# Performance work log

Measured on AMD Instinct MI355X. Metric: run time of the kernel, lower is better.

## Reference

```python
import jax, jax.numpy as jnp
import numpy as np

N_NODES = 50000
N_EDGES = 800000
IN_CH = 128
HEADS = 4
OUT_CH = 32


def setup_inputs() -> dict:
    key = jax.random.key(0)
    k1, k2, k3, k4 = jax.random.split(key, 4)
    x = jax.random.normal(k1, (N_NODES, IN_CH), dtype=jnp.float32)
    edge_index = jax.random.randint(k2, (2, N_EDGES), 0, N_NODES, dtype=jnp.int64)
    # nn.Linear weight [out, in] with xavier-uniform init
    limW = float(np.sqrt(6.0 / (IN_CH + HEADS * OUT_CH)))
    W = jax.random.uniform(k3, (HEADS * OUT_CH, IN_CH), minval=-limW, maxval=limW, dtype=jnp.float32)
    lima = float(np.sqrt(6.0 / (HEADS + 2 * OUT_CH)))
    att = jax.random.uniform(k4, (HEADS, 2 * OUT_CH), minval=-lima, maxval=lima, dtype=jnp.float32)
    bias = jnp.zeros((HEADS * OUT_CH,), dtype=jnp.float32)
    return {"x": x, "edge_index": edge_index, "W": W, "att": att, "bias": bias}


def reference(x, edge_index, W, att, bias):
    n = x.shape[0]
    heads, two_c = att.shape
    out_ch = two_c // 2
    loop = jnp.arange(n, dtype=edge_index.dtype)
    src = jnp.concatenate([edge_index[0], loop])  # [E+n]
    dst = jnp.concatenate([edge_index[1], loop])  # [E+n]
    h = (x @ W.T).reshape(n, heads, out_ch)       # [n, H, C]
    h_src = h[src]                                # [E+n, H, C]
    h_dst = h[dst]                                # [E+n, H, C]
    # e = sum over channels of att applied to [h_src || h_dst]
    e = (jnp.einsum('ehc,hc->eh', h_src, att[:, :out_ch])
         + jnp.einsum('ehc,hc->eh', h_dst, att[:, out_ch:]))  # [E+n, H]
    e = jax.nn.leaky_relu(e, negative_slope=0.2)
    # segment softmax over incoming edges per dst node
    e_max = jax.ops.segment_max(e, dst, num_segments=n)        # [n, H]
    alpha = jnp.exp(e - e_max[dst])                            # [E+n, H]
    a_sum = jax.ops.segment_sum(alpha, dst, num_segments=n)    # [n, H]
    alpha = alpha / jnp.maximum(a_sum[dst], 1e-10)
    weighted = h_src * alpha[..., None]                        # [E+n, H, C]
    out = jax.ops.segment_sum(weighted, dst, num_segments=n)   # [n, H, C]
    out = out.reshape(n, heads * out_ch)                       # concat=True
    return out + bias
```

## Files before the change

kernel.cpp:

```cpp
#include <hip/hip_runtime.h>
#include <hip/hip_bf16.h>
#include <math.h>

#define N_NODES 50000
#define N_EDGES 800000
#define IN_CH   128
#define HEADS   4
#define OUT_CH  32
#define HC      128
#define WROWS   136

#define CB_SHIFT 7
#define CB_NODES 128
#define N_CB     391
#define NBK      128
#define EPB      (N_EDGES / NBK)
#define PCAP     44
#define ND_CAP   48
#define CB_CAP   2560
#define NGB      196

typedef __attribute__((ext_vector_type(8))) short short8;
typedef __attribute__((ext_vector_type(4))) float floatx4;

__device__ __forceinline__ short f2bf(float f) {
    __hip_bfloat16 h = __float2bfloat16(f);
    return *reinterpret_cast<short*>(&h);
}

__global__ __launch_bounds__(256) void kA_fused(
    const int* __restrict__ src, const int* __restrict__ dst,
    unsigned* __restrict__ priv, int* __restrict__ cnt2,
    const float* __restrict__ x, const float* __restrict__ W,
    const float* __restrict__ att, __hip_bfloat16* __restrict__ hbuf,
    float* __restrict__ asrc, float* __restrict__ adst) {

    __shared__ short smem[128 * WROWS];

    const int tid = threadIdx.x;

    if (blockIdx.x < NBK) {
        int* lcnt = (int*)smem;
        const int blk = blockIdx.x;
        for (int i = tid; i < N_CB; i += 256) lcnt[i] = 0;
        __syncthreads();

        const int e0 = blk * EPB;
        for (int e = e0 + tid; e < e0 + EPB; e += 256) {
            int s = src[e];
            int d = dst[e];
            int cb = d >> CB_SHIFT;
            int pos = atomicAdd(&lcnt[cb], 1);
            if (pos < PCAP)
                priv[((size_t)cb * NBK + blk) * PCAP + pos] =
                    ((unsigned)(d & (CB_NODES - 1)) << 16) | (unsigned)s;
        }
        __syncthreads();
        for (int i = tid; i < N_CB; i += 256)
            cnt2[blk * N_CB + i] = min(lcnt[i], PCAP);
        return;
    }

    short* Wlds = smem;
    const int wave = tid >> 6;
    const int lane = tid & 63;
    const int col  = lane & 15;
    const int q    = lane >> 4;

    {
        int row  = tid >> 1;
        int half = tid & 1;
        const float4* Wr = (const float4*)(W + row * IN_CH + half * 64);
        short* dp = Wlds + row * WROWS + half * 64;
#pragma unroll
        for (int i = 0; i < 16; ++i) {
            float4 v = Wr[i];
            ushort4 p;
            p.x = (unsigned short)f2bf(v.x);
            p.y = (unsigned short)f2bf(v.y);
            p.z = (unsigned short)f2bf(v.z);
            p.w = (unsigned short)f2bf(v.w);
            *(ushort4*)(dp + i * 4) = p;
        }
    }

    float attS[8], attD[8];
#pragma unroll
    for (int t = 0; t < 8; ++t) {
        int base = (t >> 1) * 64 + (t & 1) * 16 + col;
        attS[t] = att[base];
        attD[t] = att[base + 32];
    }

    __syncthreads();

    const int node_base = (blockIdx.x - NBK) * 256;

    for (int it = 0; it < 4; ++it) {
        const int node0 = node_base + (it * 4 + wave) * 16;
        const int m  = node0 + col;
        const int mc = min(m, N_NODES - 1);

        floatx4 acc[8];
#pragma unroll
        for (int t = 0; t < 8; ++t) acc[t] = (floatx4){0.f, 0.f, 0.f, 0.f};

#pragma unroll
        for (int ks = 0; ks < 4; ++ks) {
            const float4* xp = (const float4*)(x + (size_t)mc * IN_CH + ks * 32 + q * 8);
            float4 v0 = xp[0];
            float4 v1 = xp[1];
            short8 af;
            af[0] = f2bf(v0.x); af[1] = f2bf(v0.y); af[2] = f2bf(v0.z); af[3] = f2bf(v0.w);
            af[4] = f2bf(v1.x); af[5] = f2bf(v1.y); af[6] = f2bf(v1.z); af[7] = f2bf(v1.w);
#pragma unroll
            for (int t = 0; t < 8; ++t) {
                const short8 bf = *(const short8*)(Wlds + (t * 16 + col) * WROWS + ks * 32 + q * 8);
                acc[t] = __builtin_amdgcn_mfma_f32_16x16x32_bf16(af, bf, acc[t], 0, 0, 0);
            }
        }

#pragma unroll
        for (int r = 0; r < 4; ++r) {
            const int node = node0 + q * 4 + r;
            const bool valid = node < N_NODES;
            float hs[4] = {0.f, 0.f, 0.f, 0.f};
            float hd[4] = {0.f, 0.f, 0.f, 0.f};
#pragma unroll
            for (int t = 0; t < 8; ++t) {
                float v = acc[t][r];
                if (valid) hbuf[(size_t)node * HC + t * 16 + col] = __float2bfloat16(v);
                hs[t >> 1] = fmaf(v, attS[t], hs[t >> 1]);
                hd[t >> 1] = fmaf(v, attD[t], hd[t >> 1]);
            }
#pragma unroll
            for (int off = 8; off; off >>= 1) {
#pragma unroll
                for (int h = 0; h < 4; ++h) {
                    hs[h] += __shfl_down(hs[h], off, 16);
                    hd[h] += __shfl_down(hd[h], off, 16);
                }
            }
            if (col == 0 && valid) {
#pragma unroll
                for (int h = 0; h < 4; ++h) {
                    asrc[node * HEADS + h] = hs[h];
                    adst[node * HEADS + h] = hd[h];
                }
            }
        }
    }
}

__global__ __launch_bounds__(256) void kc2_bin(
    const int* __restrict__ cnt2, const unsigned* __restrict__ priv,
    unsigned short* __restrict__ csr16, unsigned* __restrict__ meta) {

    __shared__ unsigned short list[CB_NODES * ND_CAP];
    __shared__ int lcnt[CB_NODES];
    __shared__ int ccnt[CB_NODES];
    __shared__ int lpre[CB_NODES];
    __shared__ int lcnt2[NBK];

    const int b   = blockIdx.x;
    const int tid = threadIdx.x;
    const int node0 = b << CB_SHIFT;
    const int nInB  = min(CB_NODES, N_NODES - node0);

    if (tid < CB_NODES) lcnt[tid] = 0;
    if (tid < NBK) lcnt2[tid] = cnt2[tid * N_CB + b];
    __syncthreads();

    const unsigned* p = priv + (size_t)b * NBK * PCAP;
    for (int idx = tid; idx < NBK * PCAP; idx += 256) {
        int blk = (idx * 5958) >> 18;
        int j   = idx - blk * PCAP;
        if (j < lcnt2[blk]) {
            unsigned ent = p[idx];
            int dl   = ent >> 16;
            int slot = atomicAdd(&lcnt[dl], 1);
            if (slot < ND_CAP) list[dl * ND_CAP + slot] = (unsigned short)(ent & 0xFFFFu);
        }
    }
    __syncthreads();

    if (tid < CB_NODES) { ccnt[tid] = min(lcnt[tid], ND_CAP); lpre[tid] = ccnt[tid]; }
    __syncthreads();
    for (int d = 1; d < CB_NODES; d <<= 1) {
        int v = (tid >= d && tid < CB_NODES) ? lpre[tid - d] : 0;
        __syncthreads();
        if (tid < CB_NODES) lpre[tid] += v;
        __syncthreads();
    }

    if (tid < nInB) {
        int cnt  = ccnt[tid];
        int excl = lpre[tid] - cnt;
        meta[node0 + tid] = (unsigned)(b * CB_CAP + excl) | ((unsigned)cnt << 24);
    }

    const int total = lpre[CB_NODES - 1];
    __syncthreads();
    for (int idx = tid; idx < total; idx += 256) {
        int n = 0;
#pragma unroll
        for (int s = 64; s; s >>= 1)
            if (idx >= lpre[n + s - 1]) n += s;
        int j = idx - (lpre[n] - ccnt[n]);
        csr16[b * CB_CAP + idx] = list[n * ND_CAP + j];
    }
}

__device__ __forceinline__ float edge_w(float t) {
    t = fmaxf(t, 0.2f * t);
    return __expf(t);
}

__global__ __launch_bounds__(256) void kb6_agg(
    const unsigned* __restrict__ meta, const unsigned short* __restrict__ csr16,
    const unsigned* __restrict__ hb, const float* __restrict__ asrc,
    const float* __restrict__ adst, const float* __restrict__ bias,
    float* __restrict__ out) {

    const int node = __builtin_amdgcn_readfirstlane(blockIdx.x * 4 + (threadIdx.x >> 6));
    if (node >= N_NODES) return;
    const int lane = threadIdx.x & 63;
    const int h    = lane >> 4;

    const unsigned mt = meta[node];
    const int cnt = (int)(mt >> 24);
    const unsigned short* p = csr16 + (mt & 0xFFFFFFu);

    const float ad = adst[node * HEADS + h];

    unsigned us = hb[node * 64 + lane];
    float wS = edge_w(asrc[node * HEADS + h] + ad);
    float ds = wS;
    float ax = wS * __uint_as_float(us << 16);
    float ay = wS * __uint_as_float(us & 0xffff0000u);

    int e = 0;
    for (; e + 3 < cnt; e += 4) {
        int s0 = p[e], s1 = p[e + 1], s2 = p[e + 2], s3 = p[e + 3];
        unsigned u0 = hb[s0 * 64 + lane];
        unsigned u1 = hb[s1 * 64 + lane];
        unsigned u2 = hb[s2 * 64 + lane];
        unsigned u3 = hb[s3 * 64 + lane];
        float w0 = edge_w(asrc[s0 * HEADS + h] + ad);
        float w1 = edge_w(asrc[s1 * HEADS + h] + ad);
        float w2 = edge_w(asrc[s2 * HEADS + h] + ad);
        float w3 = edge_w(asrc[s3 * HEADS + h] + ad);
        ds += (w0 + w1) + (w2 + w3);
        ax = fmaf(w0, __uint_as_float(u0 << 16), ax);
        ay = fmaf(w0, __uint_as_float(u0 & 0xffff0000u), ay);
        ax = fmaf(w1, __uint_as_float(u1 << 16), ax);
        ay = fmaf(w1, __uint_as_float(u1 & 0xffff0000u), ay);
        ax = fmaf(w2, __uint_as_float(u2 << 16), ax);
        ay = fmaf(w2, __uint_as_float(u2 & 0xffff0000u), ay);
        ax = fmaf(w3, __uint_as_float(u3 << 16), ax);
        ay = fmaf(w3, __uint_as_float(u3 & 0xffff0000u), ay);
    }
    for (; e < cnt; ++e) {
        int s0 = p[e];
        unsigned u0 = hb[s0 * 64 + lane];
        float w0 = edge_w(asrc[s0 * HEADS + h] + ad);
        ds += w0;
        ax = fmaf(w0, __uint_as_float(u0 << 16), ax);
        ay = fmaf(w0, __uint_as_float(u0 & 0xffff0000u), ay);
    }

    float inv = 1.0f / fmaxf(ds, 1e-10f);
    float2 b = *(const float2*)(bias + lane * 2);
    float2 o;
    o.x = ax * inv + b.x;
    o.y = ay * inv + b.y;
    *(float2*)(out + (size_t)node * HC + lane * 2) = o;
}

extern "C" void kernel_launch(void* const* d_in, const int* in_sizes, int n_in,
                              void* d_out, int out_size, void* d_ws, size_t ws_size,
                              hipStream_t stream) {
    const float* x    = (const float*)d_in[0];
    const int*   ei   = (const int*)d_in[1];
    const float* W    = (const float*)d_in[2];
    const float* att  = (const float*)d_in[3];
    const float* bias = (const float*)d_in[4];
    float* out = (float*)d_out;

    const int* src = ei;
    const int* dst = ei + N_EDGES;

    char* ws = (char*)d_ws;
    __hip_bfloat16* hbuf = (__hip_bfloat16*)ws;
    float*    asrc = (float*)(ws + 12800000);
    float*    adst = (float*)(ws + 13600000);
    unsigned* priv = (unsigned*)(ws + 14400000);
    int*      cnt2 = (int*)(ws + 23208448);
    unsigned* meta = (unsigned*)(ws + 23408640);
    unsigned short* csr16 = (unsigned short*)(ws + 23608640);

    kA_fused<<<NBK + NGB, 256, 0, stream>>>(src, dst, priv, cnt2,
                                            x, W, att, hbuf, asrc, adst);
    kc2_bin<<<N_CB, 256, 0, stream>>>(cnt2, priv, csr16, meta);
    kb6_agg<<<(N_NODES + 3) / 4, 256, 0, stream>>>(meta, csr16, (const unsigned*)hbuf,
                                                   asrc, adst, bias, out);
}
```

Before: 161.9 us.

## Split node GEMM across scatter and binning kernels, unroll aggregation by eight

The projection GEMM is split into smaller 64-node blocks (782 in total). Some run alongside the edge scatter in the first kernel and the rest run alongside the per-bucket binning in the second kernel. The aim is to balance work across the two launches and overlap compute-bound GEMM with the memory-bound binning phases. The binning kernel now places its shared arrays inside a shared smem buffer, and the aggregation loop gains an 8-wide unrolled gather for more memory-level parallelism. In exchange, each GEMM block reloads and converts W into LDS for fewer nodes, and register pressure in the aggregation loop rises.

After: 155.3 us. 1.04x faster.

```diff
diff --git a/kernel.cpp b/kernel.cpp
--- a/kernel.cpp
+++ b/kernel.cpp
@@ -18,7 +18,10 @@
 #define PCAP     44
 #define ND_CAP   48
 #define CB_CAP   2560
-#define NGB      196
+
+#define NG_TOT   782
+#define NG_A     586
+#define NG_B     (NG_TOT - NG_A)
 
 typedef __attribute__((ext_vector_type(8))) short short8;
 typedef __attribute__((ext_vector_type(4))) float floatx4;
@@ -26,6 +29,99 @@
 __device__ __forceinline__ short f2bf(float f) {
     __hip_bfloat16 h = __float2bfloat16(f);
     return *reinterpret_cast<short*>(&h);
+}
+
+__device__ __forceinline__ void gemm_role(
+    short* __restrict__ Wlds, int node_base,
+    const float* __restrict__ x, const float* __restrict__ W,
+    const float* __restrict__ att, __hip_bfloat16* __restrict__ hbuf,
+    float* __restrict__ asrc, float* __restrict__ adst) {
+
+    const int tid  = threadIdx.x;
+    const int wave = tid >> 6;
+    const int lane = tid & 63;
+    const int col  = lane & 15;
+    const int q    = lane >> 4;
+
+    {
+        int row  = tid >> 1;
+        int half = tid & 1;
+        const float4* Wr = (const float4*)(W + row * IN_CH + half * 64);
+        short* dp = Wlds + row * WROWS + half * 64;
+#pragma unroll
+        for (int i = 0; i < 16; ++i) {
+            float4 v = Wr[i];
+            ushort4 p;
+            p.x = (unsigned short)f2bf(v.x);
+            p.y = (unsigned short)f2bf(v.y);
+            p.z = (unsigned short)f2bf(v.z);
+            p.w = (unsigned short)f2bf(v.w);
+            *(ushort4*)(dp + i * 4) = p;
+        }
+    }
+
+    float attS[8], attD[8];
+#pragma unroll
+    for (int t = 0; t < 8; ++t) {
+        int base = (t >> 1) * 64 + (t & 1) * 16 + col;
+        attS[t] = att[base];
+        attD[t] = att[base + 32];
+    }
+
+    __syncthreads();
+
+    const int node0 = node_base + wave * 16;
+    const int m  = node0 + col;
+    const int mc = min(m, N_NODES - 1);
+
+    floatx4 acc[8];
+#pragma unroll
+    for (int t = 0; t < 8; ++t) acc[t] = (floatx4){0.f, 0.f, 0.f, 0.f};
+
+#pragma unroll
+    for (int ks = 0; ks < 4; ++ks) {
+        const float4* xp = (const float4*)(x + (size_t)mc * IN_CH + ks * 32 + q * 8);
+        float4 v0 = xp[0];
+        float4 v1 = xp[1];
+        short8 af;
+        af[0] = f2bf(v0.x); af[1] = f2bf(v0.y); af[2] = f2bf(v0.z); af[3] = f2bf(v0.w);
+        af[4] = f2bf(v1.x); af[5] = f2bf(v1.y); af[6] = f2bf(v1.z); af[7] = f2bf(v1.w);
+#pragma unroll
+        for (int t = 0; t < 8; ++t) {
+            const short8 bf = *(const short8*)(Wlds + (t * 16 + col) * WROWS + ks * 32 + q * 8);
+            acc[t] = __builtin_amdgcn_mfma_f32_16x16x32_bf16(af, bf, acc[t], 0, 0, 0);
+        }
+    }
+
+#pragma unroll
+    for (int r = 0; r < 4; ++r) {
+        const int node = node0 + q * 4 + r;
+        const bool valid = node < N_NODES;
+        float hs[4] = {0.f, 0.f, 0.f, 0.f};
+        float hd[4] = {0.f, 0.f, 0.f, 0.f};
+#pragma unroll
+        for (int t = 0; t < 8; ++t) {
+            float v = acc[t][r];
+            if (valid) hbuf[(size_t)node * HC + t * 16 + col] = __float2bfloat16(v);
+            hs[t >> 1] = fmaf(v, attS[t], hs[t >> 1]);
+            hd[t >> 1] = fmaf(v, attD[t], hd[t >> 1]);
+        }
+#pragma unroll
+        for (int off = 8; off; off >>= 1) {
+#pragma unroll
+            for (int h = 0; h < 4; ++h) {
+                hs[h] += __shfl_down(hs[h], off, 16);
+                hd[h] += __shfl_down(hd[h], off, 16);
+            }
+        }
+        if (col == 0 && valid) {
+#pragma unroll
+            for (int h = 0; h < 4; ++h) {
+                asrc[node * HEADS + h] = hs[h];
+                adst[node * HEADS + h] = hd[h];
+            }
+        }
+    }
 }
 
 __global__ __launch_bounds__(256) void kA_fused(
@@ -36,7 +132,6 @@
     float* __restrict__ asrc, float* __restrict__ adst) {
 
     __shared__ short smem[128 * WROWS];
-
     const int tid = threadIdx.x;
 
     if (blockIdx.x < NBK) {
@@ -61,109 +156,31 @@
         return;
     }
 
-    short* Wlds = smem;
-    const int wave = tid >> 6;
-    const int lane = tid & 63;
-    const int col  = lane & 15;
-    const int q    = lane >> 4;
-
-    {
-        int row  = tid >> 1;
-        int half = tid & 1;
-        const float4* Wr = (const float4*)(W + row * IN_CH + half * 64);
-        short* dp = Wlds + row * WROWS + half * 64;
-#pragma unroll
-        for (int i = 0; i < 16; ++i) {
-            float4 v = Wr[i];
-            ushort4 p;
-            p.x = (unsigned short)f2bf(v.x);
-            p.y = (unsigned short)f2bf(v.y);
-            p.z = (unsigned short)f2bf(v.z);
-            p.w = (unsigned short)f2bf(v.w);
-            *(ushort4*)(dp + i * 4) = p;
-        }
-    }
-
-    float attS[8], attD[8];
-#pragma unroll
-    for (int t = 0; t < 8; ++t) {
-        int base = (t >> 1) * 64 + (t & 1) * 16 + col;
-        attS[t] = att[base];
-        attD[t] = att[base + 32];
-    }
-
-    __syncthreads();
-
-    const int node_base = (blockIdx.x - NBK) * 256;
-
-    for (int it = 0; it < 4; ++it) {
-        const int node0 = node_base + (it * 4 + wave) * 16;
-        const int m  = node0 + col;
-        const int mc = min(m, N_NODES - 1);
-
-        floatx4 acc[8];
-#pragma unroll
-        for (int t = 0; t < 8; ++t) acc[t] = (floatx4){0.f, 0.f, 0.f, 0.f};
-
-#pragma unroll
-        for (int ks = 0; ks < 4; ++ks) {
-            const float4* xp = (const float4*)(x + (size_t)mc * IN_CH + ks * 32 + q * 8);
-            float4 v0 = xp[0];
-            float4 v1 = xp[1];
-            short8 af;
-            af[0] = f2bf(v0.x); af[1] = f2bf(v0.y); af[2] = f2bf(v0.z); af[3] = f2bf(v0.w);
-            af[4] = f2bf(v1.x); af[5] = f2bf(v1.y); af[6] = f2bf(v1.z); af[7] = f2bf(v1.w);
-#pragma unroll
-            for (int t = 0; t < 8; ++t) {
-                const short8 bf = *(const short8*)(Wlds + (t * 16 + col) * WROWS + ks * 32 + q * 8);
-                acc[t] = __builtin_amdgcn_mfma_f32_16x16x32_bf16(af, bf, acc[t], 0, 0, 0);
-            }
-        }
-
-#pragma unroll
-        for (int r = 0; r < 4; ++r) {
-            const int node = node0 + q * 4 + r;
-            const bool valid = node < N_NODES;
-            float hs[4] = {0.f, 0.f, 0.f, 0.f};
-            float hd[4] = {0.f, 0.f, 0.f, 0.f};
-#pragma unroll
-            for (int t = 0; t < 8; ++t) {
-                float v = acc[t][r];
-                if (valid) hbuf[(size_t)node * HC + t * 16 + col] = __float2bfloat16(v);
-                hs[t >> 1] = fmaf(v, attS[t], hs[t >> 1]);
-                hd[t >> 1] = fmaf(v, attD[t], hd[t >> 1]);
-            }
-#pragma unroll
-            for (int off = 8; off; off >>= 1) {
-#pragma unroll
-                for (int h = 0; h < 4; ++h) {
-                    hs[h] += __shfl_down(hs[h], off, 16);
-                    hd[h] += __shfl_down(hd[h], off, 16);
-                }
-            }
-            if (col == 0 && valid) {
-#pragma unroll
-                for (int h = 0; h < 4; ++h) {
-                    asrc[node * HEADS + h] = hs[h];
-                    adst[node * HEADS + h] = hd[h];
-                }
-            }
-        }
-    }
-}
-
-__global__ __launch_bounds__(256) void kc2_bin(
+    gemm_role(smem, (blockIdx.x - NBK) * 64, x, W, att, hbuf, asrc, adst);
+}
+
+__global__ __launch_bounds__(256) void kB_fused(
     const int* __restrict__ cnt2, const unsigned* __restrict__ priv,
-    unsigned short* __restrict__ csr16, unsigned* __restrict__ meta) {
-
-    __shared__ unsigned short list[CB_NODES * ND_CAP];
-    __shared__ int lcnt[CB_NODES];
-    __shared__ int ccnt[CB_NODES];
-    __shared__ int lpre[CB_NODES];
-    __shared__ int lcnt2[NBK];
-
-    const int b   = blockIdx.x;
+    unsigned short* __restrict__ csr16, unsigned* __restrict__ meta,
+    const float* __restrict__ x, const float* __restrict__ W,
+    const float* __restrict__ att, __hip_bfloat16* __restrict__ hbuf,
+    float* __restrict__ asrc, float* __restrict__ adst) {
+
+    __shared__ short smem[128 * WROWS];
     const int tid = threadIdx.x;
+
+    if (blockIdx.x >= N_CB) {
+        gemm_role(smem, (NG_A + (int)blockIdx.x - N_CB) * 64, x, W, att, hbuf, asrc, adst);
+        return;
+    }
+
+    unsigned short* list = (unsigned short*)smem;
+    int* lcnt  = (int*)(smem + 6400);
+    int* ccnt  = (int*)(smem + 6656);
+    int* lpre  = (int*)(smem + 6912);
+    int* lcnt2 = (int*)(smem + 7168);
+
+    const int b = blockIdx.x;
     const int node0 = b << CB_SHIFT;
     const int nInB  = min(CB_NODES, N_NODES - node0);
 
@@ -240,6 +257,43 @@
     float ay = wS * __uint_as_float(us & 0xffff0000u);
 
     int e = 0;
+    for (; e + 7 < cnt; e += 8) {
+        int s0 = p[e],     s1 = p[e + 1], s2 = p[e + 2], s3 = p[e + 3];
+        int s4 = p[e + 4], s5 = p[e + 5], s6 = p[e + 6], s7 = p[e + 7];
+        unsigned u0 = hb[s0 * 64 + lane];
+        unsigned u1 = hb[s1 * 64 + lane];
+        unsigned u2 = hb[s2 * 64 + lane];
+        unsigned u3 = hb[s3 * 64 + lane];
+        unsigned u4 = hb[s4 * 64 + lane];
+        unsigned u5 = hb[s5 * 64 + lane];
+        unsigned u6 = hb[s6 * 64 + lane];
+        unsigned u7 = hb[s7 * 64 + lane];
+        float w0 = edge_w(asrc[s0 * HEADS + h] + ad);
+        float w1 = edge_w(asrc[s1 * HEADS + h] + ad);
+        float w2 = edge_w(asrc[s2 * HEADS + h] + ad);
+        float w3 = edge_w(asrc[s3 * HEADS + h] + ad);
+        float w4 = edge_w(asrc[s4 * HEADS + h] + ad);
+        float w5 = edge_w(asrc[s5 * HEADS + h] + ad);
+        float w6 = edge_w(asrc[s6 * HEADS + h] + ad);
+        float w7 = edge_w(asrc[s7 * HEADS + h] + ad);
+        ds += ((w0 + w1) + (w2 + w3)) + ((w4 + w5) + (w6 + w7));
+        ax = fmaf(w0, __uint_as_float(u0 << 16), ax);
+        ay = fmaf(w0, __uint_as_float(u0 & 0xffff0000u), ay);
+        ax = fmaf(w1, __uint_as_float(u1 << 16), ax);
+        ay = fmaf(w1, __uint_as_float(u1 & 0xffff0000u), ay);
+        ax = fmaf(w2, __uint_as_float(u2 << 16), ax);
+        ay = fmaf(w2, __uint_as_float(u2 & 0xffff0000u), ay);
+        ax = fmaf(w3, __uint_as_float(u3 << 16), ax);
+        ay = fmaf(w3, __uint_as_float(u3 & 0xffff0000u), ay);
+        ax = fmaf(w4, __uint_as_float(u4 << 16), ax);
+        ay = fmaf(w4, __uint_as_float(u4 & 0xffff0000u), ay);
+        ax = fmaf(w5, __uint_as_float(u5 << 16), ax);
+        ay = fmaf(w5, __uint_as_float(u5 & 0xffff0000u), ay);
+        ax = fmaf(w6, __uint_as_float(u6 << 16), ax);
+        ay = fmaf(w6, __uint_as_float(u6 & 0xffff0000u), ay);
+        ax = fmaf(w7, __uint_as_float(u7 << 16), ax);
+        ay = fmaf(w7, __uint_as_float(u7 & 0xffff0000u), ay);
+    }
     for (; e + 3 < cnt; e += 4) {
         int s0 = p[e], s1 = p[e + 1], s2 = p[e + 2], s3 = p[e + 3];
         unsigned u0 = hb[s0 * 64 + lane];
@@ -299,9 +353,10 @@
     unsigned* meta = (unsigned*)(ws + 23408640);
     unsigned short* csr16 = (unsigned short*)(ws + 23608640);
 
-    kA_fused<<<NBK + NGB, 256, 0, stream>>>(src, dst, priv, cnt2,
-                                            x, W, att, hbuf, asrc, adst);
-    kc2_bin<<<N_CB, 256, 0, stream>>>(cnt2, priv, csr16, meta);
+    kA_fused<<<NBK + NG_A, 256, 0, stream>>>(src, dst, priv, cnt2,
+                                             x, W, att, hbuf, asrc, adst);
+    kB_fused<<<N_CB + NG_B, 256, 0, stream>>>(cnt2, priv, csr16, meta,
+                                              x, W, att, hbuf, asrc, adst);
     kb6_agg<<<(N_NODES + 3) / 4, 256, 0, stream>>>(meta, csr16, (const unsigned*)hbuf,
                                                    asrc, adst, bias, out);
 }
```

## Fold attention projections into GEMM and fuse binning with aggregation

Applied to the files above, without the earlier changes.

A new one-block prep kernel converts W to bf16 once and appends W^T·att rows, so the GEMM produces the per-head source and destination attention logits as a ninth MFMA tile instead of using shuffle reductions. The GEMM blocks now each handle 64 nodes, with more blocks and no per-block W conversion. The separate CSR build kernel is merged into the aggregation: each block bins one half of a 128-node bucket into a shared-memory list and aggregates directly from it, with the edge loop unrolled by 8. This drops a launch and the CSR and meta global round trip. In exchange, each bucket's private lists are scanned twice (once per half), and the extra prep launch is serial.

After: 174.5 us. +7.8%, slower.

```diff
diff --git a/kernel.cpp b/kernel.cpp
--- a/kernel.cpp
+++ b/kernel.cpp
@@ -17,8 +17,7 @@
 #define EPB      (N_EDGES / NBK)
 #define PCAP     44
 #define ND_CAP   48
-#define CB_CAP   2560
-#define NGB      196
+#define NG_TOT   782
 
 typedef __attribute__((ext_vector_type(8))) short short8;
 typedef __attribute__((ext_vector_type(4))) float floatx4;
@@ -28,19 +27,113 @@
     return *reinterpret_cast<short*>(&h);
 }
 
+__global__ __launch_bounds__(256) void kP_prep(
+    const float* __restrict__ W, const float* __restrict__ att,
+    unsigned short* __restrict__ Wb) {
+
+    const int tid = threadIdx.x;
+
+    {
+        int row  = tid >> 1;
+        int half = tid & 1;
+        const float4* Wr = (const float4*)(W + row * IN_CH + half * 64);
+        unsigned short* dp = Wb + row * WROWS + half * 64;
+#pragma unroll
+        for (int i = 0; i < 16; ++i) {
+            float4 v = Wr[i];
+            ushort4 p;
+            p.x = (unsigned short)f2bf(v.x);
+            p.y = (unsigned short)f2bf(v.y);
+            p.z = (unsigned short)f2bf(v.z);
+            p.w = (unsigned short)f2bf(v.w);
+            *(ushort4*)(dp + i * 4) = p;
+        }
+    }
+
+#pragma unroll
+    for (int k = 0; k < 4; ++k) {
+        int idx  = tid + k * 256;
+        int j    = idx >> 7;
+        int i    = idx & 127;
+        int head = j & 3;
+        int aoff = (j & 4) ? 32 : 0;
+        float s = 0.f;
+#pragma unroll
+        for (int c = 0; c < 32; ++c)
+            s = fmaf(W[(head * 32 + c) * IN_CH + i], att[head * 64 + aoff + c], s);
+        Wb[(128 + j) * WROWS + i] = (unsigned short)f2bf(s);
+    }
+
+    for (int z = tid; z < 8 * WROWS; z += 256) Wb[136 * WROWS + z] = 0;
+}
+
+__device__ __forceinline__ void gemm_role(
+    short* __restrict__ Wlds, int node_base,
+    const float* __restrict__ x, const unsigned short* __restrict__ Wb,
+    __hip_bfloat16* __restrict__ hbuf,
+    float* __restrict__ asrc, float* __restrict__ adst) {
+
+    const int tid  = threadIdx.x;
+    const int wave = tid >> 6;
+    const int lane = tid & 63;
+    const int col  = lane & 15;
+    const int q    = lane >> 4;
+
+#pragma unroll
+    for (int i = 0; i < 10; ++i) {
+        int off = ((i << 2) + wave) * 64 + lane;
+        ((float4*)Wlds)[off] = ((const float4*)Wb)[off];
+    }
+    __syncthreads();
+
+    const int node0 = node_base + wave * 16;
+    const int m  = node0 + col;
+    const int mc = min(m, N_NODES - 1);
+
+    floatx4 acc[9];
+#pragma unroll
+    for (int t = 0; t < 9; ++t) acc[t] = (floatx4){0.f, 0.f, 0.f, 0.f};
+
+#pragma unroll
+    for (int ks = 0; ks < 4; ++ks) {
+        const float4* xp = (const float4*)(x + (size_t)mc * IN_CH + ks * 32 + q * 8);
+        float4 v0 = xp[0];
+        float4 v1 = xp[1];
+        short8 af;
+        af[0] = f2bf(v0.x); af[1] = f2bf(v0.y); af[2] = f2bf(v0.z); af[3] = f2bf(v0.w);
+        af[4] = f2bf(v1.x); af[5] = f2bf(v1.y); af[6] = f2bf(v1.z); af[7] = f2bf(v1.w);
+#pragma unroll
+        for (int t = 0; t < 9; ++t) {
+            const short8 bf = *(const short8*)(Wlds + (t * 16 + col) * WROWS + ks * 32 + q * 8);
+            acc[t] = __builtin_amdgcn_mfma_f32_16x16x32_bf16(af, bf, acc[t], 0, 0, 0);
+        }
+    }
+
+#pragma unroll
+    for (int r = 0; r < 4; ++r) {
+        const int node = node0 + q * 4 + r;
+        if (node >= N_NODES) continue;
+#pragma unroll
+        for (int t = 0; t < 8; ++t)
+            hbuf[(size_t)node * HC + t * 16 + col] = __float2bfloat16(acc[t][r]);
+        float v8 = acc[8][r];
+        if (col < 4)      asrc[node * HEADS + col] = v8;
+        else if (col < 8) adst[node * HEADS + col - 4] = v8;
+    }
+}
+
 __global__ __launch_bounds__(256) void kA_fused(
     const int* __restrict__ src, const int* __restrict__ dst,
     unsigned* __restrict__ priv, int* __restrict__ cnt2,
-    const float* __restrict__ x, const float* __restrict__ W,
-    const float* __restrict__ att, __hip_bfloat16* __restrict__ hbuf,
+    const float* __restrict__ x, const unsigned short* __restrict__ Wb,
+    __hip_bfloat16* __restrict__ hbuf,
     float* __restrict__ asrc, float* __restrict__ adst) {
 
-    __shared__ short smem[128 * WROWS];
-
+    __shared__ float4 smem4[2560];
     const int tid = threadIdx.x;
 
     if (blockIdx.x < NBK) {
-        int* lcnt = (int*)smem;
+        int* lcnt = (int*)smem4;
         const int blk = blockIdx.x;
         for (int i = tid; i < N_CB; i += 256) lcnt[i] = 0;
         __syncthreads();
@@ -61,113 +154,32 @@
         return;
     }
 
-    short* Wlds = smem;
+    gemm_role((short*)smem4, (blockIdx.x - NBK) * 64, x, Wb, hbuf, asrc, adst);
+}
+
+__device__ __forceinline__ float edge_w(float t) {
+    t = fmaxf(t, 0.2f * t);
+    return __expf(t);
+}
+
+__global__ __launch_bounds__(256) void kD_binagg(
+    const int* __restrict__ cnt2, const unsigned* __restrict__ priv,
+    const unsigned* __restrict__ hb, const float* __restrict__ asrc,
+    const float* __restrict__ adst, const float* __restrict__ bias,
+    float* __restrict__ out) {
+
+    __shared__ unsigned short list[64 * ND_CAP];
+    __shared__ int lcnt[64];
+    __shared__ int lcnt2[NBK];
+
+    const int b    = blockIdx.x >> 1;
+    const int half = blockIdx.x & 1;
+    const int tid  = threadIdx.x;
     const int wave = tid >> 6;
     const int lane = tid & 63;
-    const int col  = lane & 15;
-    const int q    = lane >> 4;
-
-    {
-        int row  = tid >> 1;
-        int half = tid & 1;
-        const float4* Wr = (const float4*)(W + row * IN_CH + half * 64);
-        short* dp = Wlds + row * WROWS + half * 64;
-#pragma unroll
-        for (int i = 0; i < 16; ++i) {
-            float4 v = Wr[i];
-            ushort4 p;
-            p.x = (unsigned short)f2bf(v.x);
-            p.y = (unsigned short)f2bf(v.y);
-            p.z = (unsigned short)f2bf(v.z);
-            p.w = (unsigned short)f2bf(v.w);
-            *(ushort4*)(dp + i * 4) = p;
-        }
-    }
-
-    float attS[8], attD[8];
-#pragma unroll
-    for (int t = 0; t < 8; ++t) {
-        int base = (t >> 1) * 64 + (t & 1) * 16 + col;
-        attS[t] = att[base];
-        attD[t] = att[base + 32];
-    }
-
-    __syncthreads();
-
-    const int node_base = (blockIdx.x - NBK) * 256;
-
-    for (int it = 0; it < 4; ++it) {
-        const int node0 = node_base + (it * 4 + wave) * 16;
-        const int m  = node0 + col;
-        const int mc = min(m, N_NODES - 1);
-
-        floatx4 acc[8];
-#pragma unroll
-        for (int t = 0; t < 8; ++t) acc[t] = (floatx4){0.f, 0.f, 0.f, 0.f};
-
-#pragma unroll
-        for (int ks = 0; ks < 4; ++ks) {
-            const float4* xp = (const float4*)(x + (size_t)mc * IN_CH + ks * 32 + q * 8);
-            float4 v0 = xp[0];
-            float4 v1 = xp[1];
-            short8 af;
-            af[0] = f2bf(v0.x); af[1] = f2bf(v0.y); af[2] = f2bf(v0.z); af[3] = f2bf(v0.w);
-            af[4] = f2bf(v1.x); af[5] = f2bf(v1.y); af[6] = f2bf(v1.z); af[7] = f2bf(v1.w);
-#pragma unroll
-            for (int t = 0; t < 8; ++t) {
-                const short8 bf = *(const short8*)(Wlds + (t * 16 + col) * WROWS + ks * 32 + q * 8);
-                acc[t] = __builtin_amdgcn_mfma_f32_16x16x32_bf16(af, bf, acc[t], 0, 0, 0);
-            }
-        }
-
-#pragma unroll
-        for (int r = 0; r < 4; ++r) {
-            const int node = node0 + q * 4 + r;
-            const bool valid = node < N_NODES;
-            float hs[4] = {0.f, 0.f, 0.f, 0.f};
-            float hd[4] = {0.f, 0.f, 0.f, 0.f};
-#pragma unroll
-            for (int t = 0; t < 8; ++t) {
-                float v = acc[t][r];
-                if (valid) hbuf[(size_t)node * HC + t * 16 + col] = __float2bfloat16(v);
-                hs[t >> 1] = fmaf(v, attS[t], hs[t >> 1]);
-                hd[t >> 1] = fmaf(v, attD[t], hd[t >> 1]);
-            }
-#pragma unroll
-            for (int off = 8; off; off >>= 1) {
-#pragma unroll
-                for (int h = 0; h < 4; ++h) {
-                    hs[h] += __shfl_down(hs[h], off, 16);
-                    hd[h] += __shfl_down(hd[h], off, 16);
-                }
-            }
-            if (col == 0 && valid) {
-#pragma unroll
-                for (int h = 0; h < 4; ++h) {
-                    asrc[node * HEADS + h] = hs[h];
-                    adst[node * HEADS + h] = hd[h];
-                }
-            }
-        }
-    }
-}
-
-__global__ __launch_bounds__(256) void kc2_bin(
-    const int* __restrict__ cnt2, const unsigned* __restrict__ priv,
-    unsigned short* __restrict__ csr16, unsigned* __restrict__ meta) {
-
-    __shared__ unsigned short list[CB_NODES * ND_CAP];
-    __shared__ int lcnt[CB_NODES];
-    __shared__ int ccnt[CB_NODES];
-    __shared__ int lpre[CB_NODES];
-    __shared__ int lcnt2[NBK];
-
-    const int b   = blockIdx.x;
-    const int tid = threadIdx.x;
-    const int node0 = b << CB_SHIFT;
-    const int nInB  = min(CB_NODES, N_NODES - node0);
-
-    if (tid < CB_NODES) lcnt[tid] = 0;
+    const int node0 = (b << CB_SHIFT) + half * 64;
+
+    if (tid < 64) lcnt[tid] = 0;
     if (tid < NBK) lcnt2[tid] = cnt2[tid * N_CB + b];
     __syncthreads();
 
@@ -177,104 +189,86 @@
         int j   = idx - blk * PCAP;
         if (j < lcnt2[blk]) {
             unsigned ent = p[idx];
-            int dl   = ent >> 16;
-            int slot = atomicAdd(&lcnt[dl], 1);
-            if (slot < ND_CAP) list[dl * ND_CAP + slot] = (unsigned short)(ent & 0xFFFFu);
+            int dl = ent >> 16;
+            if ((dl >> 6) == half) {
+                int slot = atomicAdd(&lcnt[dl & 63], 1);
+                if (slot < ND_CAP)
+                    list[(dl & 63) * ND_CAP + slot] = (unsigned short)(ent & 0xFFFFu);
+            }
         }
     }
     __syncthreads();
 
-    if (tid < CB_NODES) { ccnt[tid] = min(lcnt[tid], ND_CAP); lpre[tid] = ccnt[tid]; }
-    __syncthreads();
-    for (int d = 1; d < CB_NODES; d <<= 1) {
-        int v = (tid >= d && tid < CB_NODES) ? lpre[tid - d] : 0;
-        __syncthreads();
-        if (tid < CB_NODES) lpre[tid] += v;
-        __syncthreads();
-    }
-
-    if (tid < nInB) {
-        int cnt  = ccnt[tid];
-        int excl = lpre[tid] - cnt;
-        meta[node0 + tid] = (unsigned)(b * CB_CAP + excl) | ((unsigned)cnt << 24);
-    }
-
-    const int total = lpre[CB_NODES - 1];
-    __syncthreads();
-    for (int idx = tid; idx < total; idx += 256) {
-        int n = 0;
-#pragma unroll
-        for (int s = 64; s; s >>= 1)
-            if (idx >= lpre[n + s - 1]) n += s;
-        int j = idx - (lpre[n] - ccnt[n]);
-        csr16[b * CB_CAP + idx] = list[n * ND_CAP + j];
-    }
-}
-
-__device__ __forceinline__ float edge_w(float t) {
-    t = fmaxf(t, 0.2f * t);
-    return __expf(t);
-}
-
-__global__ __launch_bounds__(256) void kb6_agg(
-    const unsigned* __restrict__ meta, const unsigned short* __restrict__ csr16,
-    const unsigned* __restrict__ hb, const float* __restrict__ asrc,
-    const float* __restrict__ adst, const float* __restrict__ bias,
-    float* __restrict__ out) {
-
-    const int node = __builtin_amdgcn_readfirstlane(blockIdx.x * 4 + (threadIdx.x >> 6));
-    if (node >= N_NODES) return;
-    const int lane = threadIdx.x & 63;
-    const int h    = lane >> 4;
-
-    const unsigned mt = meta[node];
-    const int cnt = (int)(mt >> 24);
-    const unsigned short* p = csr16 + (mt & 0xFFFFFFu);
-
-    const float ad = adst[node * HEADS + h];
-
-    unsigned us = hb[node * 64 + lane];
-    float wS = edge_w(asrc[node * HEADS + h] + ad);
-    float ds = wS;
-    float ax = wS * __uint_as_float(us << 16);
-    float ay = wS * __uint_as_float(us & 0xffff0000u);
-
-    int e = 0;
-    for (; e + 3 < cnt; e += 4) {
-        int s0 = p[e], s1 = p[e + 1], s2 = p[e + 2], s3 = p[e + 3];
-        unsigned u0 = hb[s0 * 64 + lane];
-        unsigned u1 = hb[s1 * 64 + lane];
-        unsigned u2 = hb[s2 * 64 + lane];
-        unsigned u3 = hb[s3 * 64 + lane];
-        float w0 = edge_w(asrc[s0 * HEADS + h] + ad);
-        float w1 = edge_w(asrc[s1 * HEADS + h] + ad);
-        float w2 = edge_w(asrc[s2 * HEADS + h] + ad);
-        float w3 = edge_w(asrc[s3 * HEADS + h] + ad);
-        ds += (w0 + w1) + (w2 + w3);
-        ax = fmaf(w0, __uint_as_float(u0 << 16), ax);
-        ay = fmaf(w0, __uint_as_float(u0 & 0xffff0000u), ay);
-        ax = fmaf(w1, __uint_as_float(u1 << 16), ax);
-        ay = fmaf(w1, __uint_as_float(u1 & 0xffff0000u), ay);
-        ax = fmaf(w2, __uint_as_float(u2 << 16), ax);
-        ay = fmaf(w2, __uint_as_float(u2 & 0xffff0000u), ay);
-        ax = fmaf(w3, __uint_as_float(u3 << 16), ax);
-        ay = fmaf(w3, __uint_as_float(u3 & 0xffff0000u), ay);
-    }
-    for (; e < cnt; ++e) {
-        int s0 = p[e];
-        unsigned u0 = hb[s0 * 64 + lane];
-        float w0 = edge_w(asrc[s0 * HEADS + h] + ad);
-        ds += w0;
-        ax = fmaf(w0, __uint_as_float(u0 << 16), ax);
-        ay = fmaf(w0, __uint_as_float(u0 & 0xffff0000u), ay);
-    }
-
-    float inv = 1.0f / fmaxf(ds, 1e-10f);
-    float2 b = *(const float2*)(bias + lane * 2);
-    float2 o;
-    o.x = ax * inv + b.x;
-    o.y = ay * inv + b.y;
-    *(float2*)(out + (size_t)node * HC + lane * 2) = o;
+    const int h = lane >> 4;
+    const float2 bv = *(const float2*)(bias + lane * 2);
+
+    for (int nn = wave; nn < 64; nn += 4) {
+        const int node = node0 + nn;
+        if (node >= N_NODES) continue;
+        const int cnt = min(lcnt[nn], ND_CAP);
+        const unsigned short* pl = &list[nn * ND_CAP];
+
+        const float ad = adst[node * HEADS + h];
+
+        unsigned us = hb[node * 64 + lane];
+        float wS = edge_w(asrc[node * HEADS + h] + ad);
+        float ds = wS;
+        float ax = wS * __uint_as_float(us << 16);
+        float ay = wS * __uint_as_float(us & 0xffff0000u);
+
+        int e = 0;
+        for (; e + 7 < cnt; e += 8) {
+            int s0 = pl[e],     s1 = pl[e + 1], s2 = pl[e + 2], s3 = pl[e + 3];
+            int s4 = pl[e + 4], s5 = pl[e + 5], s6 = pl[e + 6], s7 = pl[e + 7];
+            unsigned u0 = hb[s0 * 64 + lane];
+            unsigned u1 = hb[s1 * 64 + lane];
+            unsigned u2 = hb[s2 * 64 + lane];
+            unsigned u3 = hb[s3 * 64 + lane];
+            unsigned u4 = hb[s4 * 64 + lane];
+            unsigned u5 = hb[s5 * 64 + lane];
+            unsigned u6 = hb[s6 * 64 + lane];
+            unsigned u7 = hb[s7 * 64 + lane];
+            float w0 = edge_w(asrc[s0 * HEADS + h] + ad);
+            float w1 = edge_w(asrc[s1 * HEADS + h] + ad);
+            float w2 = edge_w(asrc[s2 * HEADS + h] + ad);
+            float w3 = edge_w(asrc[s3 * HEADS + h] + ad);
+            float w4 = edge_w(asrc[s4 * HEADS + h] + ad);
+            float w5 = edge_w(asrc[s5 * HEADS + h] + ad);
+            float w6 = edge_w(asrc[s6 * HEADS + h] + ad);
+            float w7 = edge_w(asrc[s7 * HEADS + h] + ad);
+            ds += ((w0 + w1) + (w2 + w3)) + ((w4 + w5) + (w6 + w7));
+            ax = fmaf(w0, __uint_as_float(u0 << 16), ax);
+            ay = fmaf(w0, __uint_as_float(u0 & 0xffff0000u), ay);
+            ax = fmaf(w1, __uint_as_float(u1 << 16), ax);
+            ay = fmaf(w1, __uint_as_float(u1 & 0xffff0000u), ay);
+            ax = fmaf(w2, __uint_as_float(u2 << 16), ax);
+            ay = fmaf(w2, __uint_as_float(u2 & 0xffff0000u), ay);
+            ax = fmaf(w3, __uint_as_float(u3 << 16), ax);
+            ay = fmaf(w3, __uint_as_float(u3 & 0xffff0000u), ay);
+            ax = fmaf(w4, __uint_as_float(u4 << 16), ax);
+            ay = fmaf(w4, __uint_as_float(u4 & 0xffff0000u), ay);
+            ax = fmaf(w5, __uint_as_float(u5 << 16), ax);
+            ay = fmaf(w5, __uint_as_float(u5 & 0xffff0000u), ay);
+            ax = fmaf(w6, __uint_as_float(u6 << 16), ax);
+            ay = fmaf(w6, __uint_as_float(u6 & 0xffff0000u), ay);
+            ax = fmaf(w7, __uint_as_float(u7 << 16), ax);
+            ay = fmaf(w7, __uint_as_float(u7 & 0xffff0000u), ay);
+        }
+        for (; e < cnt; ++e) {
+            int s0 = pl[e];
+            unsigned u0 = hb[s0 * 64 + lane];
+            float w0 = edge_w(asrc[s0 * HEADS + h] + ad);
+            ds += w0;
+            ax = fmaf(w0, __uint_as_float(u0 << 16), ax);
+            ay = fmaf(w0, __uint_as_float(u0 & 0xffff0000u), ay);
+        }
+
+        float inv = 1.0f / fmaxf(ds, 1e-10f);
+        float2 o;
+        o.x = ax * inv + bv.x;
+        o.y = ay * inv + bv.y;
+        *(float2*)(out + (size_t)node * HC + lane * 2) = o;
+    }
 }
 
 extern "C" void kernel_launch(void* const* d_in, const int* in_sizes, int n_in,
@@ -296,12 +290,11 @@
     float*    adst = (float*)(ws + 13600000);
     unsigned* priv = (unsigned*)(ws + 14400000);
     int*      cnt2 = (int*)(ws + 23208448);
-    unsigned* meta = (unsigned*)(ws + 23408640);
-    unsigned short* csr16 = (unsigned short*)(ws + 23608640);
-
-    kA_fused<<<NBK + NGB, 256, 0, stream>>>(src, dst, priv, cnt2,
-                                            x, W, att, hbuf, asrc, adst);
-    kc2_bin<<<N_CB, 256, 0, stream>>>(cnt2, priv, csr16, meta);
-    kb6_agg<<<(N_NODES + 3) / 4, 256, 0, stream>>>(meta, csr16, (const unsigned*)hbuf,
-                                                   asrc, adst, bias, out);
-}
+    unsigned short* Wb = (unsigned short*)(ws + 23408640);
+
+    kP_prep<<<1, 256, 0, stream>>>(W, att, Wb);
+    kA_fused<<<NBK + NG_TOT, 256, 0, stream>>>(src, dst, priv, cnt2,
+                                               x, Wb, hbuf, asrc, adst);
+    kD_binagg<<<N_CB * 2, 256, 0, stream>>>(cnt2, priv, (const unsigned*)hbuf,
+                                            asrc, adst, bias, out);
+}
```
